# Optimization experiments

Hardware: AMD Instinct MI355X
Metric: run time of the kernel (lower is better)

## Reference

```python
import jax, jax.numpy as jnp
import numpy as np
from jax import lax

# ---- static config (matches init_kwargs) ----
BATCH, SEQ, D_MODEL = 2, 512, 1024
D_STATE, EXPAND, HEADDIM, D_CONV = 64, 2, 64, 4
VNUM, HORIZON = 3, 20
D_INNER = EXPAND * D_MODEL            # 2048
NHEADS = D_INNER // HEADDIM           # 32
CONV_DIM = D_INNER + 2 * D_STATE      # x, B, C go through the depthwise conv
D_IN_PROJ = 2 * D_INNER + 2 * D_STATE + NHEADS  # z | xBC | dt
RMS_EPS = 1e-5


def setup_inputs() -> dict:
    key = jax.random.key(0)
    ks = jax.random.split(key, 10)
    s = 0.02
    return {
        "embed_data": jax.random.normal(ks[0], (BATCH, SEQ, D_MODEL), jnp.float32),
        "in_proj_w": (jax.random.normal(ks[1], (D_IN_PROJ, D_MODEL), jnp.float32) * s),
        "conv_w": (jax.random.normal(ks[2], (CONV_DIM, D_CONV), jnp.float32) * s),
        "conv_b": jnp.zeros((CONV_DIM,), jnp.float32),
        # dt_bias = softplus^{-1}(dt_init) with dt_init ~ U(1e-3, 0.1), as in Mamba2
        "dt_bias": jnp.log(jnp.expm1(jax.random.uniform(ks[3], (NHEADS,), jnp.float32, 1e-3, 0.1))),
        # A = -exp(A_log), A_init ~ U(1, 16)
        "A_log": jnp.log(jax.random.uniform(ks[4], (NHEADS,), jnp.float32, 1.0, 16.0)),
        "D": jnp.ones((NHEADS,), jnp.float32),
        "norm_w": jnp.ones((D_INNER,), jnp.float32),
        "out_proj_w": (jax.random.normal(ks[5], (D_MODEL, D_INNER), jnp.float32) * s),
        "dec_cur_w": (jax.random.normal(ks[6], (VNUM, D_MODEL), jnp.float32) * s),
        "dec_cur_b": jnp.zeros((VNUM,), jnp.float32),
        "dec_fut_w": (jax.random.normal(ks[7], (HORIZON * VNUM, D_MODEL), jnp.float32) * s),
        "dec_fut_b": jnp.zeros((HORIZON * VNUM,), jnp.float32),
    }


def _mamba2(embed_data, in_proj_w, conv_w, conv_b, dt_bias, A_log, D, norm_w, out_proj_w):
    b, s, _ = embed_data.shape
    zxbcdt = jnp.einsum('bsd,ed->bse', embed_data, in_proj_w)  # [B,S,D_IN_PROJ]
    z = zxbcdt[..., :D_INNER]
    xBC = zxbcdt[..., D_INNER:D_INNER + CONV_DIM]
    dt = zxbcdt[..., D_INNER + CONV_DIM:]                      # [B,S,H]

    # causal depthwise conv1d (kernel=4) + silu
    xpad = jnp.pad(xBC, ((0, 0), (D_CONV - 1, 0), (0, 0)))
    xBC = sum(conv_w[:, k] * xpad[:, k:k + s, :] for k in range(D_CONV)) + conv_b
    xBC = jax.nn.silu(xBC)

    x = xBC[..., :D_INNER].reshape(b, s, NHEADS, HEADDIM)       # [B,S,H,P]
    Bm = xBC[..., D_INNER:D_INNER + D_STATE]                    # [B,S,N]
    Cm = xBC[..., D_INNER + D_STATE:]                           # [B,S,N]

    dt = jax.nn.softplus(dt + dt_bias)                          # [B,S,H]
    A = -jnp.exp(A_log)                                         # [H]

    # selective state-space scan: h_t = exp(dt*A) h_{t-1} + dt * x_t B_t^T
    def step(h, inp):
        x_t, dt_t, b_t, c_t = inp                               # [B,H,P],[B,H],[B,N],[B,N]
        dA = jnp.exp(dt_t * A)                                  # [B,H]
        h = h * dA[..., None, None] + (dt_t[..., None] * x_t)[..., None] * b_t[:, None, None, :]
        y = jnp.einsum('bhpn,bn->bhp', h, c_t)
        return h, y

    h0 = jnp.zeros((b, NHEADS, HEADDIM, D_STATE), embed_data.dtype)
    xs = (x.transpose(1, 0, 2, 3), dt.transpose(1, 0, 2),
          Bm.transpose(1, 0, 2), Cm.transpose(1, 0, 2))
    _, ys = lax.scan(step, h0, xs)                              # [S,B,H,P]
    y = ys.transpose(1, 0, 2, 3) + D[None, None, :, None] * x   # skip term D*x
    y = y.reshape(b, s, D_INNER)

    # gated RMSNorm: rmsnorm(y * silu(z)) * w
    y = y * jax.nn.silu(z)
    y = y * lax.rsqrt(jnp.mean(y * y, axis=-1, keepdims=True) + RMS_EPS) * norm_w
    return jnp.einsum('bsi,di->bsd', y, out_proj_w)             # [B,S,D_MODEL]


def reference(embed_data, in_proj_w, conv_w, conv_b, dt_bias, A_log, D, norm_w,
              out_proj_w, dec_cur_w, dec_cur_b, dec_fut_w, dec_fut_b):
    h = _mamba2(embed_data, in_proj_w, conv_w, conv_b, dt_bias, A_log, D, norm_w, out_proj_w)
    pred_current = jnp.einsum('bsd,vd->bsv', h, dec_cur_w) + dec_cur_b         # [B,S,V]
    pred_future = (h[:, -1] @ dec_fut_w.T + dec_fut_b).reshape(h.shape[0], HORIZON, VNUM)
    return (pred_current, pred_future)
```

## Files before the change

### kernel.cpp

```cpp
#include <hip/hip_runtime.h>
#include <hip/hip_bf16.h>

#define BATCH   2
#define SEQ     512
#define DMODEL  1024
#define DSTATE  64
#define HEADDIM 64
#define DCONV   4
#define VNUM    3
#define HORIZON 20
#define DINNER  2048
#define NHEADS  32
#define CONVDIM 2176
#define DINPROJ 4256
#define NPAD1   4352
#define BS      (BATCH*SEQ)
#define RMS_EPS 1e-5f
#define CHUNK   64
#define NCHUNK  (SEQ/CHUNK)
#define NDEC    (VNUM + HORIZON*VNUM)
#define WC_DS   32

typedef __attribute__((ext_vector_type(8))) short bf16x8;
typedef __attribute__((ext_vector_type(4))) float f32x4;

__device__ __forceinline__ unsigned short f2b(float x) {
    union { float f; unsigned u; } v; v.f = x;
    return (unsigned short)((v.u + 0x7fffu + ((v.u >> 16) & 1u)) >> 16);
}

__device__ __forceinline__ float silu(float x) { return x / (1.f + expf(-x)); }

__device__ __forceinline__ void async16(const void* g, const void* l) {
    __builtin_amdgcn_global_load_lds(
        (const __attribute__((address_space(1))) unsigned int*)g,
        (__attribute__((address_space(3))) unsigned int*)l, 16, 0, 0);
}

template<int BM, int BN, int FM, int FN, int KD>
__global__ __launch_bounds__(256) void gemm_bf16(const short* __restrict__ A,
                                                 const short* __restrict__ B,
                                                 float* __restrict__ C, int N) {
    constexpr int WM = FM * 16, WN = FN * 16;
    static_assert(BM == 2 * WM && BN == 2 * WN, "2x2 waves");
    __shared__ __align__(16) short At[BM * 32];
    __shared__ __align__(16) short Bt[BN * 32];
    const int t    = threadIdx.x;
    const int lane = t & 63;
    const int w    = t >> 6;
    const int wm   = (w >> 1) * WM, wn = (w & 1) * WN;
    const int row0 = blockIdx.y * BM, col0 = blockIdx.x * BN;
    const int fr   = lane & 15;
    const int kq   = lane >> 4;
    const int lr   = t >> 2;
    const int lc   = (t & 3) * 8;

    const short* Ag = A + (size_t)(row0 + lr) * KD + lc;
    const short* Bg = B + (size_t)(col0 + lr) * KD + lc;

    f32x4 acc[FM][FN];
#pragma unroll
    for (int i = 0; i < FM; ++i)
#pragma unroll
        for (int j = 0; j < FN; ++j)
#pragma unroll
            for (int r = 0; r < 4; ++r) acc[i][j][r] = 0.f;

    for (int k0 = 0; k0 < KD; k0 += 32) {
        __syncthreads();
#pragma unroll
        for (int i = 0; i < BM / 64; ++i)
            async16(Ag + (size_t)i * 64 * KD + k0, (const char*)At + i * 4096 + t * 16);
#pragma unroll
        for (int i = 0; i < BN / 64; ++i)
            async16(Bg + (size_t)i * 64 * KD + k0, (const char*)Bt + i * 4096 + t * 16);
        __syncthreads();

        bf16x8 af[FM], bv[FN];
#pragma unroll
        for (int i = 0; i < FM; ++i)
            af[i] = *(const bf16x8*)&At[(wm + i * 16 + fr) * 32 + kq * 8];
#pragma unroll
        for (int j = 0; j < FN; ++j)
            bv[j] = *(const bf16x8*)&Bt[(wn + j * 16 + fr) * 32 + kq * 8];
#pragma unroll
        for (int i = 0; i < FM; ++i)
#pragma unroll
            for (int j = 0; j < FN; ++j)
                acc[i][j] = __builtin_amdgcn_mfma_f32_16x16x32_bf16(
                    af[i], bv[j], acc[i][j], 0, 0, 0);
    }

    const int orow = lane >> 4;
#pragma unroll
    for (int i = 0; i < FM; ++i)
#pragma unroll
        for (int j = 0; j < FN; ++j) {
            const int col = col0 + wn + j * 16 + fr;
            if (col < N) {
#pragma unroll
                for (int r = 0; r < 4; ++r) {
                    const int row = row0 + wm + i * 16 + orow * 4 + r;
                    C[(size_t)row * N + col] = acc[i][j][r];
                }
            }
        }
}

#define EMB4     (BS * DMODEL / 4)
#define IPW4     (NPAD1 * DMODEL / 4)
#define CASTBLKS ((EMB4 + IPW4) / 256)
__global__ __launch_bounds__(256) void prep_kernel(
        const float* __restrict__ embed, const float* __restrict__ ipw,
        short* __restrict__ embB, short* __restrict__ ipwB,
        const float* __restrict__ op, const float* __restrict__ cwv,
        const float* __restrict__ fwv, float* __restrict__ P) {
    __shared__ float lw[32][64];
    if (blockIdx.x < CASTBLKS) {
        const int i = blockIdx.x * 256 + threadIdx.x;
        if (i < EMB4) {
            float4 v = *(const float4*)(embed + (size_t)i * 4);
            *(short4*)(embB + (size_t)i * 4) =
                make_short4((short)f2b(v.x), (short)f2b(v.y),
                            (short)f2b(v.z), (short)f2b(v.w));
        } else {
            const int j = i - EMB4;
            const size_t e0 = (size_t)j * 4;
            const int row = (int)(e0 / DMODEL);
            short4 o;
            if (row < DINPROJ) {
                float4 v = *(const float4*)(ipw + e0);
                o = make_short4((short)f2b(v.x), (short)f2b(v.y),
                                (short)f2b(v.z), (short)f2b(v.w));
            } else {
                o = make_short4(0, 0, 0, 0);
            }
            *(short4*)(ipwB + e0) = o;
        }
        return;
    }
    const int blk   = blockIdx.x - CASTBLKS;
    const int itile = blk & 7;
    const int ds    = blk >> 3;
    const int i     = itile * 256 + threadIdx.x;
    const int d0    = ds * 32;

#pragma unroll
    for (int k = 0; k < 8; ++k) {
        const int e = threadIdx.x * 8 + k;
        const int d = e >> 6, v = e & 63;
        float val = 0.f;
        if (v < VNUM)      val = cwv[(size_t)v * DMODEL + d0 + d];
        else if (v < NDEC) val = fwv[(size_t)(v - VNUM) * DMODEL + d0 + d];
        lw[d][v] = val;
    }

    float opc[32];
#pragma unroll
    for (int d = 0; d < 32; ++d) opc[d] = op[(size_t)(d0 + d) * DINNER + i];
    __syncthreads();

    f32x4 acc[16];
#pragma unroll
    for (int q = 0; q < 16; ++q)
#pragma unroll
        for (int r = 0; r < 4; ++r) acc[q][r] = 0.f;

#pragma unroll
    for (int d = 0; d < 32; ++d) {
        const float o = opc[d];
#pragma unroll
        for (int q = 0; q < 16; ++q) {
            float4 wv = *(const float4*)&lw[d][q * 4];
            acc[q][0] += o * wv.x; acc[q][1] += o * wv.y;
            acc[q][2] += o * wv.z; acc[q][3] += o * wv.w;
        }
    }

    float* Pp = P + (size_t)ds * 64 * DINNER + i;
#pragma unroll
    for (int q = 0; q < 16; ++q)
#pragma unroll
        for (int r = 0; r < 4; ++r)
            Pp[(size_t)(q * 4 + r) * DINNER] = acc[q][r];
}

#define CONVBLKS (BS * CONVDIM / 4 / 256)
__global__ __launch_bounds__(256) void conv_kernel(
        const float* __restrict__ zxbcdt, const float* __restrict__ cw,
        const float* __restrict__ cb, float* __restrict__ xbc) {
    const int item = blockIdx.x * 256 + threadIdx.x;
    const int c4 = item % (CONVDIM / 4);
    const int rs = item / (CONVDIM / 4);
    const int s  = rs % SEQ;
    const int c  = c4 * 4;
    const float* src = zxbcdt + (size_t)rs * DINPROJ + DINNER + c;
    float4 x0 = (s >= 3) ? *(const float4*)(src - 3 * DINPROJ) : make_float4(0,0,0,0);
    float4 x1 = (s >= 2) ? *(const float4*)(src - 2 * DINPROJ) : make_float4(0,0,0,0);
    float4 x2 = (s >= 1) ? *(const float4*)(src - 1 * DINPROJ) : make_float4(0,0,0,0);
    float4 x3 = *(const float4*)(src);
    float4 bias = *(const float4*)(cb + c);
    float4 r;
    { float4 w = *(const float4*)(cw + (size_t)(c+0)*4);
      r.x = bias.x + w.x*x0.x + w.y*x1.x + w.z*x2.x + w.w*x3.x; }
    { float4 w = *(const float4*)(cw + (size_t)(c+1)*4);
      r.y = bias.y + w.x*x0.y + w.y*x1.y + w.z*x2.y + w.w*x3.y; }
    { float4 w = *(const float4*)(cw + (size_t)(c+2)*4);
      r.z = bias.z + w.x*x0.z + w.y*x1.z + w.z*x2.z + w.w*x3.z; }
    { float4 w = *(const float4*)(cw + (size_t)(c+3)*4);
      r.w = bias.w + w.x*x0.w + w.y*x1.w + w.z*x2.w + w.w*x3.w; }
    r.x = silu(r.x); r.y = silu(r.y); r.z = silu(r.z); r.w = silu(r.w);
    *(float4*)(xbc + (size_t)rs * CONVDIM + c) = r;
}

__global__ __launch_bounds__(256) void chunk_intra_kernel(
        const float* __restrict__ zx, const float* __restrict__ xbc,
        const float* __restrict__ dt_bias, const float* __restrict__ A_log,
        const float* __restrict__ Dv, float* __restrict__ yraw,
        float* __restrict__ Sc, float* __restrict__ dexp) {
    const int blk = blockIdx.x;
    const int c  = blk & 7;
    const int bh = blk >> 3;
    const int h  = bh & 31;
    const int b  = bh >> 5;
    const int rs0 = b * SEQ + c * CHUNK;

    __shared__ float sBn[64][68];
    __shared__ float sX [64][68];
    __shared__ float sMT[64][68];
    __shared__ float sl[64], se[64], sdt[64];

    const int tid = threadIdx.x;
    const float A = -expf(A_log[h]);

    if (tid < 64) {
        const float raw = zx[(size_t)(rs0 + tid) * DINPROJ + DINNER + CONVDIM + h]
                          + dt_bias[h];
        const float dtv = fmaxf(raw, 0.f) + log1pf(expf(-fabsf(raw)));
        sdt[tid] = dtv;
        float v = dtv * A;
#pragma unroll
        for (int off = 1; off < 64; off <<= 1) {
            float o = __shfl_up(v, off, 64);
            if (tid >= off) v += o;
        }
        sl[tid] = v;
        const float ltot = __shfl(v, 63, 64);
        se[tid] = expf(ltot - v);
        dexp[(size_t)blk * 64 + tid] = expf(v);
    }

    {
        const int row = tid >> 2;
        const int cq  = tid & 3;
        const float* xrow = xbc + (size_t)(rs0 + row) * CONVDIM;
#pragma unroll
        for (int i = 0; i < 4; ++i) {
            const int n = cq * 16 + i * 4;
            float4 bv = *(const float4*)(xrow + DINNER + n);
            float4 cv = *(const float4*)(xrow + DINNER + DSTATE + n);
            sBn[n+0][row] = bv.x; sBn[n+1][row] = bv.y;
            sBn[n+2][row] = bv.z; sBn[n+3][row] = bv.w;
            sX [n+0][row] = cv.x; sX [n+1][row] = cv.y;
            sX [n+2][row] = cv.z; sX [n+3][row] = cv.w;
        }
    }
    __syncthreads();

    const int g0 = (tid >> 4) * 4;
    const int g1 = (tid & 15) * 4;

    {
        const int t0 = g0, s0 = g1;
        float acc[4][4] = {};
        for (int n = 0; n < 64; ++n) {
            float4 ct = *(const float4*)&sX [n][t0];
            float4 bs = *(const float4*)&sBn[n][s0];
            float cta[4] = {ct.x, ct.y, ct.z, ct.w};
            float bsa[4] = {bs.x, bs.y, bs.z, bs.w};
#pragma unroll
            for (int i = 0; i < 4; ++i)
#pragma unroll
                for (int j = 0; j < 4; ++j) acc[i][j] += cta[i] * bsa[j];
        }
#pragma unroll
        for (int i = 0; i < 4; ++i) {
            const int t = t0 + i;
            const float lt = sl[t];
#pragma unroll
            for (int j = 0; j < 4; ++j) {
                const int s = s0 + j;
                sMT[s][t] = (s <= t) ? expf(lt - sl[s]) * acc[i][j] : 0.f;
            }
        }
    }
    __syncthreads();

    {
        const int row = tid >> 2;
        const int cq  = tid & 3;
        const float* xrow = xbc + (size_t)(rs0 + row) * CONVDIM + h * HEADDIM;
        const float dtv = sdt[row];
#pragma unroll
        for (int i = 0; i < 4; ++i) {
            const int p = cq * 16 + i * 4;
            float4 xv = *(const float4*)(xrow + p);
            sX[row][p+0] = dtv * xv.x; sX[row][p+1] = dtv * xv.y;
            sX[row][p+2] = dtv * xv.z; sX[row][p+3] = dtv * xv.w;
        }
    }
    __syncthreads();

    {
        const int t0 = g0, p0 = g1;
        float acc[4][4] = {};
        for (int s = 0; s < 64; ++s) {
            float4 mt = *(const float4*)&sMT[s][t0];
            float4 us = *(const float4*)&sX [s][p0];
            float mta[4] = {mt.x, mt.y, mt.z, mt.w};
            float usa[4] = {us.x, us.y, us.z, us.w};
#pragma unroll
            for (int i = 0; i < 4; ++i)
#pragma unroll
                for (int j = 0; j < 4; ++j) acc[i][j] += mta[i] * usa[j];
        }
        const float Dh = Dv[h];
#pragma unroll
        for (int i = 0; i < 4; ++i) {
            const int t = t0 + i;
            const float dr = Dh / sdt[t];
            float4 uv = *(const float4*)&sX[t][p0];
            float4 yv = make_float4(acc[i][0] + dr * uv.x, acc[i][1] + dr * uv.y,
                                    acc[i][2] + dr * uv.z, acc[i][3] + dr * uv.w);
            *(float4*)&yraw[(size_t)(rs0 + t) * DINNER + h * HEADDIM + p0] = yv;
        }
    }

    {
        const int p0 = g0, n0 = g1;
        float acc[4][4] = {};
        for (int s = 0; s < 64; ++s) {
            const float es = se[s];
            float4 up = *(const float4*)&sX[s][p0];
            float upa[4] = {es * up.x, es * up.y, es * up.z, es * up.w};
            float bna[4] = {sBn[n0+0][s], sBn[n0+1][s], sBn[n0+2][s], sBn[n0+3][s]};
#pragma unroll
            for (int i = 0; i < 4; ++i)
#pragma unroll
                for (int j = 0; j < 4; ++j) acc[i][j] += upa[i] * bna[j];
        }
        float* scp = Sc + (size_t)blk * (HEADDIM * DSTATE);
#pragma unroll
        for (int i = 0; i < 4; ++i) {
            float4 v = make_float4(acc[i][0], acc[i][1], acc[i][2], acc[i][3]);
            *(float4*)&scp[(size_t)(p0 + i) * DSTATE + n0] = v;
        }
    }
}

__global__ __launch_bounds__(256) void comb_reduce_kernel(
        const float* __restrict__ Sc, const float* __restrict__ dexp,
        float* __restrict__ h0ws, const float* __restrict__ P,
        float* __restrict__ W) {
    if (blockIdx.x < 256) {
        const int bh = blockIdx.x >> 2;
        const int e  = (blockIdx.x & 3) * 1024 + threadIdx.x * 4;
        float4 h = make_float4(0.f, 0.f, 0.f, 0.f);
        for (int c = 0; c < NCHUNK; ++c) {
            const size_t base = (size_t)(bh * NCHUNK + c) * (HEADDIM * DSTATE);
            const float ac = dexp[(size_t)(bh * NCHUNK + c) * 64 + 63];
            *(float4*)&h0ws[base + e] = h;
            float4 s = *(const float4*)&Sc[base + e];
            h.x = ac * h.x + s.x; h.y = ac * h.y + s.y;
            h.z = ac * h.z + s.z; h.w = ac * h.w + s.w;
        }
    } else {
        const int idx = (blockIdx.x - 256) * 256 + threadIdx.x;
        float s = 0.f;
#pragma unroll
        for (int ds = 0; ds < WC_DS; ++ds) s += P[(size_t)ds * 64 * DINNER + idx];
        W[idx] = s;
    }
}

__global__ __launch_bounds__(256) void chunk_state_out_kernel(
        const float* __restrict__ xbc, const float* __restrict__ h0ws,
        const float* __restrict__ dexp, float* __restrict__ yraw) {
    const int blk = blockIdx.x;
    const int c  = blk & 7;
    if (c == 0) return;
    const int bh = blk >> 3;
    const int h  = bh & 31;
    const int b  = bh >> 5;
    const int rs0 = b * SEQ + c * CHUNK;

    __shared__ float sCn[64][68];
    __shared__ float sH [64][68];
    __shared__ float sdex[64];
    const int tid = threadIdx.x;
    {
        const int row = tid >> 2;
        const int cq  = tid & 3;
        const float* xrow = xbc + (size_t)(rs0 + row) * CONVDIM + DINNER + DSTATE;
        const float* hrow = h0ws + (size_t)blk * (HEADDIM * DSTATE)
                            + (size_t)row * DSTATE;
#pragma unroll
        for (int i = 0; i < 4; ++i) {
            const int n = cq * 16 + i * 4;
            float4 cv = *(const float4*)(xrow + n);
            float4 hv = *(const float4*)(hrow + n);
            sCn[n+0][row] = cv.x; sCn[n+1][row] = cv.y;
            sCn[n+2][row] = cv.z; sCn[n+3][row] = cv.w;
            sH [n+0][row] = hv.x; sH [n+1][row] = hv.y;
            sH [n+2][row] = hv.z; sH [n+3][row] = hv.w;
        }
    }
    if (tid < 64) sdex[tid] = dexp[(size_t)blk * 64 + tid];
    __syncthreads();

    const int t0 = (tid >> 4) * 4;
    const int p0 = (tid & 15) * 4;
    float acc[4][4] = {};
    for (int n = 0; n < 64; ++n) {
        float4 ct = *(const float4*)&sCn[n][t0];
        float4 hp = *(const float4*)&sH [n][p0];
        float cta[4] = {ct.x, ct.y, ct.z, ct.w};
        float hpa[4] = {hp.x, hp.y, hp.z, hp.w};
#pragma unroll
        for (int i = 0; i < 4; ++i)
#pragma unroll
            for (int j = 0; j < 4; ++j) acc[i][j] += cta[i] * hpa[j];
    }
#pragma unroll
    for (int i = 0; i < 4; ++i) {
        const float d = sdex[t0 + i];
        float* yp = &yraw[(size_t)(rs0 + t0 + i) * DINNER + h * HEADDIM + p0];
        float4 old = *(const float4*)yp;
        *(float4*)yp = make_float4(old.x + d * acc[i][0], old.y + d * acc[i][1],
                                   old.z + d * acc[i][2], old.w + d * acc[i][3]);
    }
}

__global__ __launch_bounds__(256) void gate_norm_pred_kernel(
        const float* __restrict__ zxbcdt, const float* __restrict__ y,
        const float* __restrict__ nw, const float* __restrict__ W,
        const float* __restrict__ cur_b, float* __restrict__ out,
        float* __restrict__ ylast) {
    const int rs = blockIdx.x;
    const int t  = threadIdx.x;
    const float* z  = zxbcdt + (size_t)rs * DINPROJ;
    const float* yr = y + (size_t)rs * DINNER;

    float vals[8];
    float ss = 0.f;
#pragma unroll
    for (int i = 0; i < 8; ++i) {
        const int c = t + i * 256;
        const float zv = z[c];
        const float v  = yr[c] * (zv / (1.f + expf(-zv)));
        vals[i] = v;
        ss += v * v;
    }
#pragma unroll
    for (int off = 32; off > 0; off >>= 1) ss += __shfl_down(ss, off, 64);
    __shared__ float red[4];
    if ((t & 63) == 0) red[t >> 6] = ss;
    __syncthreads();
    const float tot   = red[0] + red[1] + red[2] + red[3];
    const float scale = rsqrtf(tot / (float)DINNER + RMS_EPS);

    const bool is_last = ((rs & (SEQ - 1)) == SEQ - 1);
    float p0 = 0.f, p1 = 0.f, p2 = 0.f;
#pragma unroll
    for (int i = 0; i < 8; ++i) {
        const int c = t + i * 256;
        const float vn = vals[i] * scale * nw[c];
        vals[i] = vn;
        p0 += vn * W[c];
        p1 += vn * W[DINNER + c];
        p2 += vn * W[2 * DINNER + c];
    }
    if (is_last) {
        float* yl = ylast + (size_t)(rs >> 9) * DINNER;
#pragma unroll
        for (int i = 0; i < 8; ++i) yl[t + i * 256] = vals[i];
    }
#pragma unroll
    for (int off = 32; off > 0; off >>= 1) {
        p0 += __shfl_down(p0, off, 64);
        p1 += __shfl_down(p1, off, 64);
        p2 += __shfl_down(p2, off, 64);
    }
    __shared__ float r3[4][3];
    if ((t & 63) == 0) { r3[t >> 6][0] = p0; r3[t >> 6][1] = p1; r3[t >> 6][2] = p2; }
    __syncthreads();
    if (t < VNUM) {
        const float s = r3[0][t] + r3[1][t] + r3[2][t] + r3[3][t];
        out[(size_t)rs * VNUM + t] = s + cur_b[t];
    }
}

__global__ __launch_bounds__(256) void pred_fut_kernel(
        const float* __restrict__ ylast, const float* __restrict__ W,
        const float* __restrict__ bvec, float* __restrict__ out) {
    const int blk = blockIdx.x;
    const int b = blk / (HORIZON * VNUM);
    const int j = blk % (HORIZON * VNUM);
    const float* yl = ylast + (size_t)b * DINNER;
    const float* wr = W + (size_t)(VNUM + j) * DINNER;
    float pv = 0.f;
    for (int i = threadIdx.x; i < DINNER; i += 256) pv += yl[i] * wr[i];
#pragma unroll
    for (int off = 32; off > 0; off >>= 1) pv += __shfl_down(pv, off, 64);
    __shared__ float red[4];
    if ((threadIdx.x & 63) == 0) red[threadIdx.x >> 6] = pv;
    __syncthreads();
    if (threadIdx.x == 0)
        out[b * (HORIZON * VNUM) + j] = red[0] + red[1] + red[2] + red[3] + bvec[j];
}

extern "C" void kernel_launch(void* const* d_in, const int* in_sizes, int n_in,
                              void* d_out, int out_size, void* d_ws, size_t ws_size,
                              hipStream_t stream) {
    const float* embed      = (const float*)d_in[0];
    const float* in_proj_w  = (const float*)d_in[1];
    const float* conv_w     = (const float*)d_in[2];
    const float* conv_b     = (const float*)d_in[3];
    const float* dt_bias    = (const float*)d_in[4];
    const float* A_log      = (const float*)d_in[5];
    const float* Dv         = (const float*)d_in[6];
    const float* norm_w     = (const float*)d_in[7];
    const float* out_proj_w = (const float*)d_in[8];
    const float* dec_cur_w  = (const float*)d_in[9];
    const float* dec_cur_b  = (const float*)d_in[10];
    const float* dec_fut_w  = (const float*)d_in[11];
    const float* dec_fut_b  = (const float*)d_in[12];

    float* ws     = (float*)d_ws;
    float* zxbcdt = ws;
    float* xbc    = zxbcdt + (size_t)BS * DINPROJ;
    float* yraw   = xbc    + (size_t)BS * CONVDIM;
    float* Sc     = yraw   + (size_t)BS * DINNER;
    float* h0ws   = Sc     + (size_t)BATCH*NHEADS*NCHUNK*HEADDIM*DSTATE;
    float* dexp   = h0ws   + (size_t)BATCH*NHEADS*NCHUNK*HEADDIM*DSTATE;
    float* Wp     = dexp   + (size_t)BATCH*NHEADS*NCHUNK*64;
    float* W      = Wp     + (size_t)WC_DS * 64 * DINNER;
    float* ylast  = W      + (size_t)64 * DINNER;
    short* embB   = (short*)(ylast + (size_t)BATCH * DINNER);
    short* ipwB   = embB + (size_t)BS * DMODEL;

    float* out = (float*)d_out;

    prep_kernel<<<CASTBLKS + 8 * WC_DS, 256, 0, stream>>>(
        embed, in_proj_w, embB, ipwB, out_proj_w, dec_cur_w, dec_fut_w, Wp);

    gemm_bf16<128, 64, 4, 2, DMODEL>
        <<<dim3(NPAD1 / 64, BS / 128), 256, 0, stream>>>(embB, ipwB, zxbcdt, DINPROJ);

    conv_kernel<<<CONVBLKS, 256, 0, stream>>>(zxbcdt, conv_w, conv_b, xbc);

    chunk_intra_kernel<<<BATCH * NHEADS * NCHUNK, 256, 0, stream>>>(
        zxbcdt, xbc, dt_bias, A_log, Dv, yraw, Sc, dexp);

    comb_reduce_kernel<<<256 + 64 * DINNER / 256, 256, 0, stream>>>(
        Sc, dexp, h0ws, Wp, W);

    chunk_state_out_kernel<<<BATCH * NHEADS * NCHUNK, 256, 0, stream>>>(
        xbc, h0ws, dexp, yraw);

    gate_norm_pred_kernel<<<BS, 256, 0, stream>>>(zxbcdt, yraw, norm_w, W,
                                                  dec_cur_b, out, ylast);

    pred_fut_kernel<<<BATCH * HORIZON * VNUM, 256, 0, stream>>>(ylast, W, dec_fut_b,
                                                                out + BS * VNUM);
}
```

Baseline: 186.2 us.

## Fold inter-chunk state scan into state-output kernel and merge W reduction into conv

Removes the separate comb_reduce kernel. The chunk-to-chunk state recurrence is now recomputed inside chunk_state_out_kernel as a weighted sum of earlier chunk states, using decay-product coefficients, so the h0ws buffer is never written or read. The weight-partials reduction moves into the conv kernel as extra blocks. This saves one launch and a 4 MB round trip, but adds redundant reads of Sc: chunk c reads c prior states, which is quadratic in the chunk count.

```diff
diff --git a/kernel.cpp b/kernel.cpp
--- a/kernel.cpp
+++ b/kernel.cpp
@@ -186,9 +186,19 @@
 }
 
 #define CONVBLKS (BS * CONVDIM / 4 / 256)
-__global__ __launch_bounds__(256) void conv_kernel(
+#define WREDBLKS (64 * DINNER / 256)
+__global__ __launch_bounds__(256) void conv_wred_kernel(
         const float* __restrict__ zxbcdt, const float* __restrict__ cw,
-        const float* __restrict__ cb, float* __restrict__ xbc) {
+        const float* __restrict__ cb, float* __restrict__ xbc,
+        const float* __restrict__ P, float* __restrict__ W) {
+    if (blockIdx.x >= CONVBLKS) {
+        const int idx = (blockIdx.x - CONVBLKS) * 256 + threadIdx.x;
+        float s = 0.f;
+#pragma unroll
+        for (int ds = 0; ds < WC_DS; ++ds) s += P[(size_t)ds * 64 * DINNER + idx];
+        W[idx] = s;
+        return;
+    }
     const int item = blockIdx.x * 256 + threadIdx.x;
     const int c4 = item % (CONVDIM / 4);
     const int rs = item / (CONVDIM / 4);
@@ -358,33 +368,8 @@
     }
 }
 
-__global__ __launch_bounds__(256) void comb_reduce_kernel(
-        const float* __restrict__ Sc, const float* __restrict__ dexp,
-        float* __restrict__ h0ws, const float* __restrict__ P,
-        float* __restrict__ W) {
-    if (blockIdx.x < 256) {
-        const int bh = blockIdx.x >> 2;
-        const int e  = (blockIdx.x & 3) * 1024 + threadIdx.x * 4;
-        float4 h = make_float4(0.f, 0.f, 0.f, 0.f);
-        for (int c = 0; c < NCHUNK; ++c) {
-            const size_t base = (size_t)(bh * NCHUNK + c) * (HEADDIM * DSTATE);
-            const float ac = dexp[(size_t)(bh * NCHUNK + c) * 64 + 63];
-            *(float4*)&h0ws[base + e] = h;
-            float4 s = *(const float4*)&Sc[base + e];
-            h.x = ac * h.x + s.x; h.y = ac * h.y + s.y;
-            h.z = ac * h.z + s.z; h.w = ac * h.w + s.w;
-        }
-    } else {
-        const int idx = (blockIdx.x - 256) * 256 + threadIdx.x;
-        float s = 0.f;
-#pragma unroll
-        for (int ds = 0; ds < WC_DS; ++ds) s += P[(size_t)ds * 64 * DINNER + idx];
-        W[idx] = s;
-    }
-}
-
 __global__ __launch_bounds__(256) void chunk_state_out_kernel(
-        const float* __restrict__ xbc, const float* __restrict__ h0ws,
+        const float* __restrict__ xbc, const float* __restrict__ Sc,
         const float* __restrict__ dexp, float* __restrict__ yraw) {
     const int blk = blockIdx.x;
     const int c  = blk & 7;
@@ -398,21 +383,37 @@
     __shared__ float sH [64][68];
     __shared__ float sdex[64];
     const int tid = threadIdx.x;
+
+    float coeff[7];
+    {
+        float prod = 1.f;
+        coeff[c - 1] = 1.f;
+        for (int k = c - 1; k >= 1; --k) {
+            prod *= dexp[(size_t)(bh * NCHUNK + k) * 64 + 63];
+            coeff[k - 1] = prod;
+        }
+    }
+
     {
         const int row = tid >> 2;
         const int cq  = tid & 3;
         const float* xrow = xbc + (size_t)(rs0 + row) * CONVDIM + DINNER + DSTATE;
-        const float* hrow = h0ws + (size_t)blk * (HEADDIM * DSTATE)
+        const float* scb  = Sc + (size_t)(bh * NCHUNK) * (HEADDIM * DSTATE)
                             + (size_t)row * DSTATE;
 #pragma unroll
         for (int i = 0; i < 4; ++i) {
             const int n = cq * 16 + i * 4;
             float4 cv = *(const float4*)(xrow + n);
-            float4 hv = *(const float4*)(hrow + n);
+            float hx = 0.f, hy = 0.f, hz = 0.f, hw = 0.f;
+            for (int cc = 0; cc < c; ++cc) {
+                float4 s = *(const float4*)(scb + (size_t)cc * (HEADDIM * DSTATE) + n);
+                const float k = coeff[cc];
+                hx += k * s.x; hy += k * s.y; hz += k * s.z; hw += k * s.w;
+            }
             sCn[n+0][row] = cv.x; sCn[n+1][row] = cv.y;
             sCn[n+2][row] = cv.z; sCn[n+3][row] = cv.w;
-            sH [n+0][row] = hv.x; sH [n+1][row] = hv.y;
-            sH [n+2][row] = hv.z; sH [n+3][row] = hv.w;
+            sH [n+0][row] = hx; sH [n+1][row] = hy;
+            sH [n+2][row] = hz; sH [n+3][row] = hw;
         }
     }
     if (tid < 64) sdex[tid] = dexp[(size_t)blk * 64 + tid];
@@ -541,8 +542,7 @@
     float* xbc    = zxbcdt + (size_t)BS * DINPROJ;
     float* yraw   = xbc    + (size_t)BS * CONVDIM;
     float* Sc     = yraw   + (size_t)BS * DINNER;
-    float* h0ws   = Sc     + (size_t)BATCH*NHEADS*NCHUNK*HEADDIM*DSTATE;
-    float* dexp   = h0ws   + (size_t)BATCH*NHEADS*NCHUNK*HEADDIM*DSTATE;
+    float* dexp   = Sc     + (size_t)BATCH*NHEADS*NCHUNK*HEADDIM*DSTATE;
     float* Wp     = dexp   + (size_t)BATCH*NHEADS*NCHUNK*64;
     float* W      = Wp     + (size_t)WC_DS * 64 * DINNER;
     float* ylast  = W      + (size_t)64 * DINNER;
@@ -557,16 +557,14 @@
     gemm_bf16<128, 64, 4, 2, DMODEL>
         <<<dim3(NPAD1 / 64, BS / 128), 256, 0, stream>>>(embB, ipwB, zxbcdt, DINPROJ);
 
-    conv_kernel<<<CONVBLKS, 256, 0, stream>>>(zxbcdt, conv_w, conv_b, xbc);
+    conv_wred_kernel<<<CONVBLKS + WREDBLKS, 256, 0, stream>>>(
+        zxbcdt, conv_w, conv_b, xbc, Wp, W);
 
     chunk_intra_kernel<<<BATCH * NHEADS * NCHUNK, 256, 0, stream>>>(
         zxbcdt, xbc, dt_bias, A_log, Dv, yraw, Sc, dexp);
 
-    comb_reduce_kernel<<<256 + 64 * DINNER / 256, 256, 0, stream>>>(
-        Sc, dexp, h0ws, Wp, W);
-
     chunk_state_out_kernel<<<BATCH * NHEADS * NCHUNK, 256, 0, stream>>>(
-        xbc, h0ws, dexp, yraw);
+        xbc, Sc, dexp, yraw);
 
     gate_norm_pred_kernel<<<BS, 256, 0, stream>>>(zxbcdt, yraw, norm_w, W,
                                                   dec_cur_b, out, ylast);
```

New measurement: 205.8 us. 10.6% more time.

## Use bf16 MFMA for chunked SSD intra-chunk and state-output matmuls

Applied to the files above, without the earlier changes.

Replaces the scalar fp32 FMA loops in chunk_intra_kernel and chunk_state_out_kernel with bf16 MFMA 16x16x32 instructions. Operands are converted to bf16 and staged in padded shared-memory tiles in row and transposed layouts. The precomputed exp-weighted U operand and a direct D*x skip read replace the old recomputation. This trades fp32 precision for matrix-core throughput, and the output stores become scalar, strided writes instead of float4 writes.

```diff
diff --git a/kernel.cpp b/kernel.cpp
--- a/kernel.cpp
+++ b/kernel.cpp
@@ -20,6 +20,7 @@
 #define NCHUNK  (SEQ/CHUNK)
 #define NDEC    (VNUM + HORIZON*VNUM)
 #define WC_DS   32
+#define LDB     72
 
 typedef __attribute__((ext_vector_type(8))) short bf16x8;
 typedef __attribute__((ext_vector_type(4))) float f32x4;
@@ -225,13 +226,43 @@
     const int b  = bh >> 5;
     const int rs0 = b * SEQ + c * CHUNK;
 
-    __shared__ float sBn[64][68];
-    __shared__ float sX [64][68];
-    __shared__ float sMT[64][68];
+    __shared__ __align__(16) short sB [64 * LDB];
+    __shared__ __align__(16) short sCt[64 * LDB];
+    __shared__ __align__(16) short sBn[64 * LDB];
+    __shared__ __align__(16) short sUt[64 * LDB];
+    __shared__ __align__(16) short sUe[64 * LDB];
+    __shared__ __align__(16) short sM [64 * LDB];
     __shared__ float sl[64], se[64], sdt[64];
 
-    const int tid = threadIdx.x;
-    const float A = -expf(A_log[h]);
+    const int tid  = threadIdx.x;
+    const int lane = tid & 63;
+    const int w    = tid >> 6;
+    const int fr   = lane & 15;
+    const int kq   = lane >> 4;
+    const int wm   = w * 16;
+    const float A  = -expf(A_log[h]);
+
+    {
+        const int row = tid >> 2;
+        const int cq  = tid & 3;
+        const float* xrow = xbc + (size_t)(rs0 + row) * CONVDIM + DINNER;
+#pragma unroll
+        for (int i = 0; i < 4; ++i) {
+            const int n = cq * 16 + i * 4;
+            float4 bv = *(const float4*)(xrow + n);
+            float4 cv = *(const float4*)(xrow + DSTATE + n);
+            short4 bs = make_short4((short)f2b(bv.x), (short)f2b(bv.y),
+                                    (short)f2b(bv.z), (short)f2b(bv.w));
+            short4 cs = make_short4((short)f2b(cv.x), (short)f2b(cv.y),
+                                    (short)f2b(cv.z), (short)f2b(cv.w));
+            *(short4*)&sB [row * LDB + n] = bs;
+            *(short4*)&sCt[row * LDB + n] = cs;
+            sBn[(n+0) * LDB + row] = bs.x;
+            sBn[(n+1) * LDB + row] = bs.y;
+            sBn[(n+2) * LDB + row] = bs.z;
+            sBn[(n+3) * LDB + row] = bs.w;
+        }
+    }
 
     if (tid < 64) {
         const float raw = zx[(size_t)(rs0 + tid) * DINPROJ + DINNER + CONVDIM + h]
@@ -249,112 +280,112 @@
         se[tid] = expf(ltot - v);
         dexp[(size_t)blk * 64 + tid] = expf(v);
     }
+    __syncthreads();
+
+    f32x4 accM[4];
+#pragma unroll
+    for (int j = 0; j < 4; ++j)
+#pragma unroll
+        for (int r = 0; r < 4; ++r) accM[j][r] = 0.f;
+#pragma unroll
+    for (int k0 = 0; k0 < 64; k0 += 32) {
+        bf16x8 af = *(const bf16x8*)&sCt[(wm + fr) * LDB + kq * 8 + k0];
+#pragma unroll
+        for (int j = 0; j < 4; ++j) {
+            bf16x8 bv = *(const bf16x8*)&sB[(j * 16 + fr) * LDB + kq * 8 + k0];
+            accM[j] = __builtin_amdgcn_mfma_f32_16x16x32_bf16(af, bv, accM[j], 0, 0, 0);
+        }
+    }
+    {
+        const int t0 = wm + kq * 4;
+        const float lt0 = sl[t0+0], lt1 = sl[t0+1], lt2 = sl[t0+2], lt3 = sl[t0+3];
+#pragma unroll
+        for (int j = 0; j < 4; ++j) {
+            const int s = j * 16 + fr;
+            const float ls = sl[s];
+            sM[(t0+0)*LDB + s] = (short)f2b((s <= t0+0) ? expf(lt0-ls)*accM[j][0] : 0.f);
+            sM[(t0+1)*LDB + s] = (short)f2b((s <= t0+1) ? expf(lt1-ls)*accM[j][1] : 0.f);
+            sM[(t0+2)*LDB + s] = (short)f2b((s <= t0+2) ? expf(lt2-ls)*accM[j][2] : 0.f);
+            sM[(t0+3)*LDB + s] = (short)f2b((s <= t0+3) ? expf(lt3-ls)*accM[j][3] : 0.f);
+        }
+    }
 
     {
         const int row = tid >> 2;
         const int cq  = tid & 3;
-        const float* xrow = xbc + (size_t)(rs0 + row) * CONVDIM;
-#pragma unroll
-        for (int i = 0; i < 4; ++i) {
-            const int n = cq * 16 + i * 4;
-            float4 bv = *(const float4*)(xrow + DINNER + n);
-            float4 cv = *(const float4*)(xrow + DINNER + DSTATE + n);
-            sBn[n+0][row] = bv.x; sBn[n+1][row] = bv.y;
-            sBn[n+2][row] = bv.z; sBn[n+3][row] = bv.w;
-            sX [n+0][row] = cv.x; sX [n+1][row] = cv.y;
-            sX [n+2][row] = cv.z; sX [n+3][row] = cv.w;
-        }
-    }
-    __syncthreads();
-
-    const int g0 = (tid >> 4) * 4;
-    const int g1 = (tid & 15) * 4;
-
-    {
-        const int t0 = g0, s0 = g1;
-        float acc[4][4] = {};
-        for (int n = 0; n < 64; ++n) {
-            float4 ct = *(const float4*)&sX [n][t0];
-            float4 bs = *(const float4*)&sBn[n][s0];
-            float cta[4] = {ct.x, ct.y, ct.z, ct.w};
-            float bsa[4] = {bs.x, bs.y, bs.z, bs.w};
-#pragma unroll
-            for (int i = 0; i < 4; ++i)
-#pragma unroll
-                for (int j = 0; j < 4; ++j) acc[i][j] += cta[i] * bsa[j];
-        }
-#pragma unroll
-        for (int i = 0; i < 4; ++i) {
-            const int t = t0 + i;
-            const float lt = sl[t];
-#pragma unroll
-            for (int j = 0; j < 4; ++j) {
-                const int s = s0 + j;
-                sMT[s][t] = (s <= t) ? expf(lt - sl[s]) * acc[i][j] : 0.f;
-            }
-        }
-    }
-    __syncthreads();
-
-    {
-        const int row = tid >> 2;
-        const int cq  = tid & 3;
-        const float* xrow = xbc + (size_t)(rs0 + row) * CONVDIM + h * HEADDIM;
         const float dtv = sdt[row];
+        const float sev = se[row];
+        const float* xr = xbc + (size_t)(rs0 + row) * CONVDIM + h * HEADDIM;
 #pragma unroll
         for (int i = 0; i < 4; ++i) {
             const int p = cq * 16 + i * 4;
-            float4 xv = *(const float4*)(xrow + p);
-            sX[row][p+0] = dtv * xv.x; sX[row][p+1] = dtv * xv.y;
-            sX[row][p+2] = dtv * xv.z; sX[row][p+3] = dtv * xv.w;
+            float4 xv = *(const float4*)(xr + p);
+            const float u0 = dtv * xv.x, u1 = dtv * xv.y;
+            const float u2 = dtv * xv.z, u3 = dtv * xv.w;
+            sUt[(p+0)*LDB + row] = (short)f2b(u0);
+            sUt[(p+1)*LDB + row] = (short)f2b(u1);
+            sUt[(p+2)*LDB + row] = (short)f2b(u2);
+            sUt[(p+3)*LDB + row] = (short)f2b(u3);
+            sUe[(p+0)*LDB + row] = (short)f2b(u0 * sev);
+            sUe[(p+1)*LDB + row] = (short)f2b(u1 * sev);
+            sUe[(p+2)*LDB + row] = (short)f2b(u2 * sev);
+            sUe[(p+3)*LDB + row] = (short)f2b(u3 * sev);
         }
     }
     __syncthreads();
 
+    f32x4 accY[4];
+#pragma unroll
+    for (int j = 0; j < 4; ++j)
+#pragma unroll
+        for (int r = 0; r < 4; ++r) accY[j][r] = 0.f;
+#pragma unroll
+    for (int k0 = 0; k0 < 64; k0 += 32) {
+        bf16x8 af = *(const bf16x8*)&sM[(wm + fr) * LDB + kq * 8 + k0];
+#pragma unroll
+        for (int j = 0; j < 4; ++j) {
+            bf16x8 bv = *(const bf16x8*)&sUt[(j * 16 + fr) * LDB + kq * 8 + k0];
+            accY[j] = __builtin_amdgcn_mfma_f32_16x16x32_bf16(af, bv, accY[j], 0, 0, 0);
+        }
+    }
+    f32x4 accS[4];
+#pragma unroll
+    for (int j = 0; j < 4; ++j)
+#pragma unroll
+        for (int r = 0; r < 4; ++r) accS[j][r] = 0.f;
+#pragma unroll
+    for (int k0 = 0; k0 < 64; k0 += 32) {
+        bf16x8 af = *(const bf16x8*)&sUe[(wm + fr) * LDB + kq * 8 + k0];
+#pragma unroll
+        for (int j = 0; j < 4; ++j) {
+            bf16x8 bv = *(const bf16x8*)&sBn[(j * 16 + fr) * LDB + kq * 8 + k0];
+            accS[j] = __builtin_amdgcn_mfma_f32_16x16x32_bf16(af, bv, accS[j], 0, 0, 0);
+        }
+    }
+
     {
-        const int t0 = g0, p0 = g1;
-        float acc[4][4] = {};
-        for (int s = 0; s < 64; ++s) {
-            float4 mt = *(const float4*)&sMT[s][t0];
-            float4 us = *(const float4*)&sX [s][p0];
-            float mta[4] = {mt.x, mt.y, mt.z, mt.w};
-            float usa[4] = {us.x, us.y, us.z, us.w};
-#pragma unroll
-            for (int i = 0; i < 4; ++i)
-#pragma unroll
-                for (int j = 0; j < 4; ++j) acc[i][j] += mta[i] * usa[j];
-        }
         const float Dh = Dv[h];
-#pragma unroll
-        for (int i = 0; i < 4; ++i) {
-            const int t = t0 + i;
-            const float dr = Dh / sdt[t];
-            float4 uv = *(const float4*)&sX[t][p0];
-            float4 yv = make_float4(acc[i][0] + dr * uv.x, acc[i][1] + dr * uv.y,
-                                    acc[i][2] + dr * uv.z, acc[i][3] + dr * uv.w);
-            *(float4*)&yraw[(size_t)(rs0 + t) * DINNER + h * HEADDIM + p0] = yv;
-        }
-    }
-
+        const int t0 = wm + kq * 4;
+#pragma unroll
+        for (int r = 0; r < 4; ++r) {
+            const int t = t0 + r;
+            const float* xr = xbc + (size_t)(rs0 + t) * CONVDIM + h * HEADDIM;
+            float* yr = yraw + (size_t)(rs0 + t) * DINNER + h * HEADDIM;
+#pragma unroll
+            for (int j = 0; j < 4; ++j) {
+                const int p = j * 16 + fr;
+                yr[p] = accY[j][r] + Dh * xr[p];
+            }
+        }
+    }
     {
-        const int p0 = g0, n0 = g1;
-        float acc[4][4] = {};
-        for (int s = 0; s < 64; ++s) {
-            const float es = se[s];
-            float4 up = *(const float4*)&sX[s][p0];
-            float upa[4] = {es * up.x, es * up.y, es * up.z, es * up.w};
-            float bna[4] = {sBn[n0+0][s], sBn[n0+1][s], sBn[n0+2][s], sBn[n0+3][s]};
-#pragma unroll
-            for (int i = 0; i < 4; ++i)
-#pragma unroll
-                for (int j = 0; j < 4; ++j) acc[i][j] += upa[i] * bna[j];
-        }
         float* scp = Sc + (size_t)blk * (HEADDIM * DSTATE);
-#pragma unroll
-        for (int i = 0; i < 4; ++i) {
-            float4 v = make_float4(acc[i][0], acc[i][1], acc[i][2], acc[i][3]);
-            *(float4*)&scp[(size_t)(p0 + i) * DSTATE + n0] = v;
-        }
+        const int p0 = wm + kq * 4;
+#pragma unroll
+        for (int r = 0; r < 4; ++r)
+#pragma unroll
+            for (int j = 0; j < 4; ++j)
+                scp[(size_t)(p0 + r) * DSTATE + j * 16 + fr] = accS[j][r];
     }
 }
 
@@ -394,10 +425,16 @@
     const int b  = bh >> 5;
     const int rs0 = b * SEQ + c * CHUNK;
 
-    __shared__ float sCn[64][68];
-    __shared__ float sH [64][68];
+    __shared__ __align__(16) short sCt[64 * LDB];
+    __shared__ __align__(16) short sH [64 * LDB];
     __shared__ float sdex[64];
-    const int tid = threadIdx.x;
+
+    const int tid  = threadIdx.x;
+    const int lane = tid & 63;
+    const int w    = tid >> 6;
+    const int fr   = lane & 15;
+    const int kq   = lane >> 4;
+    const int wm   = w * 16;
     {
         const int row = tid >> 2;
         const int cq  = tid & 3;
@@ -409,35 +446,42 @@
             const int n = cq * 16 + i * 4;
             float4 cv = *(const float4*)(xrow + n);
             float4 hv = *(const float4*)(hrow + n);
-            sCn[n+0][row] = cv.x; sCn[n+1][row] = cv.y;
-            sCn[n+2][row] = cv.z; sCn[n+3][row] = cv.w;
-            sH [n+0][row] = hv.x; sH [n+1][row] = hv.y;
-            sH [n+2][row] = hv.z; sH [n+3][row] = hv.w;
+            *(short4*)&sCt[row * LDB + n] =
+                make_short4((short)f2b(cv.x), (short)f2b(cv.y),
+                            (short)f2b(cv.z), (short)f2b(cv.w));
+            *(short4*)&sH[row * LDB + n] =
+                make_short4((short)f2b(hv.x), (short)f2b(hv.y),
+                            (short)f2b(hv.z), (short)f2b(hv.w));
         }
     }
     if (tid < 64) sdex[tid] = dexp[(size_t)blk * 64 + tid];
     __syncthreads();
 
-    const int t0 = (tid >> 4) * 4;
-    const int p0 = (tid & 15) * 4;
-    float acc[4][4] = {};
-    for (int n = 0; n < 64; ++n) {
-        float4 ct = *(const float4*)&sCn[n][t0];
-        float4 hp = *(const float4*)&sH [n][p0];
-        float cta[4] = {ct.x, ct.y, ct.z, ct.w};
-        float hpa[4] = {hp.x, hp.y, hp.z, hp.w};
-#pragma unroll
-        for (int i = 0; i < 4; ++i)
-#pragma unroll
-            for (int j = 0; j < 4; ++j) acc[i][j] += cta[i] * hpa[j];
-    }
-#pragma unroll
-    for (int i = 0; i < 4; ++i) {
-        const float d = sdex[t0 + i];
-        float* yp = &yraw[(size_t)(rs0 + t0 + i) * DINNER + h * HEADDIM + p0];
-        float4 old = *(const float4*)yp;
-        *(float4*)yp = make_float4(old.x + d * acc[i][0], old.y + d * acc[i][1],
-                                   old.z + d * acc[i][2], old.w + d * acc[i][3]);
+    f32x4 acc[4];
+#pragma unroll
+    for (int j = 0; j < 4; ++j)
+#pragma unroll
+        for (int r = 0; r < 4; ++r) acc[j][r] = 0.f;
+#pragma unroll
+    for (int k0 = 0; k0 < 64; k0 += 32) {
+        bf16x8 af = *(const bf16x8*)&sCt[(wm + fr) * LDB + kq * 8 + k0];
+#pragma unroll
+        for (int j = 0; j < 4; ++j) {
+            bf16x8 bv = *(const bf16x8*)&sH[(j * 16 + fr) * LDB + kq * 8 + k0];
+            acc[j] = __builtin_amdgcn_mfma_f32_16x16x32_bf16(af, bv, acc[j], 0, 0, 0);
+        }
+    }
+    const int t0 = wm + kq * 4;
+#pragma unroll
+    for (int r = 0; r < 4; ++r) {
+        const int t = t0 + r;
+        const float d = sdex[t];
+        float* yr = yraw + (size_t)(rs0 + t) * DINNER + h * HEADDIM;
+#pragma unroll
+        for (int j = 0; j < 4; ++j) {
+            const int p = j * 16 + fr;
+            yr[p] += d * acc[j][r];
+        }
     }
 }
 
```

Result: faster. 176.8 us (median of 2 runs) (-5.0%).
